# Kernel tuning notes

Measured on AMD Instinct MI355X. Metric: run time of the kernel, lower is better.

The kernel has to match this reference:

```python
import jax, jax.numpy as jnp
import numpy as np

NCAPS, NHIDDEN, NLAYER, ROUTIT = 8, 16, 2, 6
CUT = 5


def _normalize(v, axis):
    return v / jnp.maximum(jnp.linalg.norm(v, axis=axis, keepdims=True), 1e-12)


def _routing(x, nb_flat, k, max_iter, last):
    # x: [n, d] flat features, nb_flat: [n*m] neighbor ids (-1 = pad)
    n, d = x.shape
    dd = d // k
    m = nb_flat.shape[0] // n
    x3 = _normalize(x.reshape(n, k, dd), axis=2)              # [n,k,dd]
    x_c = jnp.concatenate([x3.reshape(n, d), jnp.zeros((1, d), x.dtype)], 0)  # [n+1,d]
    nbm = jnp.where(nb_flat < 0, n, nb_flat)
    z = x_c[nbm].reshape(n, m, k, dd)                         # neighbor gather
    u = None
    p = None
    for it in range(max_iter):
        p = jnp.zeros((n, m, k), x.dtype) if u is None else jnp.einsum('nmkc,nkc->nmk', z, u)
        p = jax.nn.softmax(p, axis=2)
        u = jnp.einsum('nmkc,nmk->nkc', z, p) + x3
        if it < max_iter - 1:
            u = _normalize(u, axis=2)
    if not last:
        return u.reshape(n, d)
    # meta-path aggregation (last layer)
    nb2 = nb_flat.reshape(n, m)
    nei_mask = (nb2 >= 0).astype(x.dtype)
    p1 = jnp.argmax(p, axis=2)                                # [n,m]
    A = jax.nn.one_hot(p1, k, dtype=x.dtype) * nei_mask[:, :, None]  # [n,m,k]
    Ai = A.transpose(2, 0, 1).astype(jnp.int32)               # [k,n,m]
    B = Ai * nb2[None].astype(jnp.int32) + (Ai - 1)           # nb where assigned, else -1
    B = jnp.concatenate([B, -jnp.ones((k, 1, m), jnp.int32)], axis=1)  # [k,n+1,m]
    mapB = jnp.where(B < 0, n, B)                             # -1 -> zero row n
    sel = mapB[:, :, :CUT]                                    # [k,n+1,CUT]
    x_c3 = x_c.reshape(n + 1, k, dd)
    gather_j = jax.vmap(lambda idx, xj: xj[idx], in_axes=(0, 1))  # over capsule j
    metas = []
    for i in range(k):
        # two-hop neighbors through capsule i then capsule j
        tmp = mapB[:, sel[i].reshape(-1), :CUT].reshape(k, n + 1, CUT * CUT)[:, :n]  # [k,n,25]
        hj = gather_j(tmp, x_c3)                               # [k,n,25,dd]
        metas.append(hj.mean(axis=2))                          # [k,n,dd]
    meta = jnp.stack(metas, 0)                                 # [i,j,n,dd]
    meta = meta.sum(axis=1).transpose(1, 0, 2)                 # sum over j -> [n,k,dd]
    meta = u + meta
    return u.reshape(n, d), meta.reshape(n, d)


def setup_inputs() -> dict:
    key = jax.random.key(0)
    ks = jax.random.split(key, 10)
    n, nfeat, nclass = 20000, 500, 16
    m = 32
    d = NCAPS * NHIDDEN
    return {
        'x': jax.random.normal(ks[0], (n, nfeat), jnp.float32),
        'nb': jax.random.randint(ks[1], (n, m), 0, n, jnp.int64),
        'pca_w': jax.random.normal(ks[2], (nfeat, d), jnp.float32) * 0.05,
        'pca_b': jax.random.normal(ks[3], (d,), jnp.float32) * 0.05,
        'ln_g': jnp.ones((NHIDDEN,), jnp.float32),
        'ln_b': jnp.zeros((NHIDDEN,), jnp.float32),
        'w_qs': jax.random.normal(ks[4], (NHIDDEN, NHIDDEN), jnp.float32) * 0.1,
        'w_ks': jax.random.normal(ks[5], (NHIDDEN, NHIDDEN), jnp.float32) * 0.1,
        'mlp_w': jax.random.normal(ks[6], (d, nclass), jnp.float32) * 0.05,
        'mlp_b': jax.random.normal(ks[7], (nclass,), jnp.float32) * 0.05,
    }


def reference(x, nb, pca_w, pca_b, ln_g, ln_b, w_qs, w_ks, mlp_w, mlp_b):
    k, dd = NCAPS, NHIDDEN
    n = x.shape[0]
    nb_flat = nb.reshape(-1)
    h = x @ pca_w + pca_b                                      # [n, d]
    h3 = h.reshape(n, k, dd)
    # Independence attention over capsules (only attn matters; output q is discarded)
    mu = h3.mean(-1, keepdims=True)
    var = ((h3 - mu) ** 2).mean(-1, keepdims=True)
    q = (h3 - mu) / jnp.sqrt(var + 1e-6) * ln_g + ln_b
    q = q @ w_qs                                               # [n,k,dd]
    kk = h3 @ w_ks
    temp = jnp.asarray(dd, x.dtype) ** 0.5
    attn = jax.nn.softmax(jnp.einsum('nqc,nkc->nqk', q / temp, kk), axis=-1)  # [n,k,k]
    off = 1.0 - jnp.eye(k, dtype=x.dtype)
    attn_loss = (attn * off).sum() / (off.sum() * n)
    h = jax.nn.relu(h3).reshape(n, k * dd)
    meta = None
    for layer in range(NLAYER):
        last = layer == NLAYER - 1
        if last:
            u, meta = _routing(h, nb_flat, k, ROUTIT, True)
        else:
            h = jax.nn.relu(_routing(h, nb_flat, k, ROUTIT, False))
    meta = jax.nn.relu(meta) @ mlp_w + mlp_b
    return jax.nn.log_softmax(meta, axis=1), attn_loss, meta
```

## Files before the change

kernel.cpp:

```cpp
#include <hip/hip_runtime.h>
#include <math.h>

#define NCAPS 8
#define DD    16
#define D     128
#define M     32
#define ROUTIT 6
#define CUT   5

__device__ __forceinline__ float wred16_sum(float v) {
    v += __shfl_xor(v, 1);
    v += __shfl_xor(v, 2);
    v += __shfl_xor(v, 4);
    v += __shfl_xor(v, 8);
    return v;
}

__device__ __forceinline__ void wave_sync_lds() {
    asm volatile("s_waitcnt lgkmcnt(0)" ::: "memory");
}

__device__ __forceinline__ void bar_lgkm() {
    asm volatile("s_waitcnt lgkmcnt(0)" ::: "memory");
    __builtin_amdgcn_s_barrier();
    asm volatile("" ::: "memory");
}

typedef _Float16 h2 __attribute__((ext_vector_type(2)));
union U32H2 { unsigned u; h2 h; };
__device__ __forceinline__ unsigned pack_h2(float a, float b) {
    U32H2 r; r.h.x = (_Float16)a; r.h.y = (_Float16)b; return r.u;
}
__device__ __forceinline__ h2 ash2(unsigned u) { U32H2 r; r.u = u; return r.h; }

__global__ __launch_bounds__(256) void pca_attn(
        const float* __restrict__ x, const float* __restrict__ w,
        const float* __restrict__ bias, const float* __restrict__ ln_g,
        const float* __restrict__ ln_b, const float* __restrict__ w_qs,
        const float* __restrict__ w_ks, unsigned* __restrict__ xc0H,
        unsigned* __restrict__ xc1H, float* __restrict__ partial,
        int n, int nfeat) {
    __shared__ alignas(16) unsigned char uS[20480];
    unsigned (*xs2)[36]  = (unsigned(*)[36])uS;
    unsigned (*ws2)[128] = (unsigned(*)[128])(uS + 1440);
    float (*ks)[8][20]   = (float(*)[8][20])uS;
    __shared__ alignas(16) float hs[32][132];
    __shared__ float wq[256], wk[256];
    __shared__ float red[4];
    const int tid = threadIdx.x;
    const int cg = tid & 31;
    const int rg = tid >> 5;
    const int row0 = blockIdx.x * 32;
    wq[tid] = w_qs[tid];
    wk[tid] = w_ks[tid];
    const float4 bi4 = *(const float4*)&bias[cg * 4];
    if (blockIdx.x == 0 && tid < 64) {
        xc0H[(size_t)n * 64 + tid] = 0u;
        xc1H[(size_t)n * 64 + tid] = 0u;
    }

    const int xr_r = tid / 5, xr_cf = tid % 5;
    const int wk0 = tid >> 5, wc0 = tid & 31;
    float4 xr{}, w0a{}, w0b{}, w1a{}, w1b{};

    {
        if (tid < 160) {
            int row = row0 + xr_r;
            xr = (row < n) ? *(const float4*)&x[(size_t)row * nfeat + xr_cf * 4]
                           : make_float4(0.f, 0.f, 0.f, 0.f);
        }
        w0a = *(const float4*)&w[(size_t)(2 * wk0) * 128 + wc0 * 4];
        w0b = *(const float4*)&w[(size_t)(2 * wk0 + 1) * 128 + wc0 * 4];
        if (tid < 64) {
            int kkp = 8 + (tid >> 5);
            w1a = *(const float4*)&w[(size_t)(2 * kkp) * 128 + wc0 * 4];
            w1b = *(const float4*)&w[(size_t)(2 * kkp + 1) * 128 + wc0 * 4];
        }
    }
    float acc[4][4] = {};
    const int ntile = nfeat / 20;
    for (int t = 0; t < ntile; ++t) {
        bar_lgkm();
        if (tid < 160) {
            xs2[xr_cf * 2 + 0][xr_r] = pack_h2(xr.x, xr.y);
            xs2[xr_cf * 2 + 1][xr_r] = pack_h2(xr.z, xr.w);
        }
        {
            uint4 pw;
            pw.x = pack_h2(w0a.x, w0b.x); pw.y = pack_h2(w0a.y, w0b.y);
            pw.z = pack_h2(w0a.z, w0b.z); pw.w = pack_h2(w0a.w, w0b.w);
            *(uint4*)&ws2[wk0][wc0 * 4] = pw;
        }
        if (tid < 64) {
            int kkp = 8 + (tid >> 5);
            uint4 pw;
            pw.x = pack_h2(w1a.x, w1b.x); pw.y = pack_h2(w1a.y, w1b.y);
            pw.z = pack_h2(w1a.z, w1b.z); pw.w = pack_h2(w1a.w, w1b.w);
            *(uint4*)&ws2[kkp][wc0 * 4] = pw;
        }
        if (t < ntile - 1) {
            int k0 = (t + 1) * 20;
            if (tid < 160) {
                int row = row0 + xr_r;
                xr = (row < n)
                    ? *(const float4*)&x[(size_t)row * nfeat + k0 + xr_cf * 4]
                    : make_float4(0.f, 0.f, 0.f, 0.f);
            }
            w0a = *(const float4*)&w[(size_t)(k0 + 2 * wk0) * 128 + wc0 * 4];
            w0b = *(const float4*)&w[(size_t)(k0 + 2 * wk0 + 1) * 128 + wc0 * 4];
            if (tid < 64) {
                int kkp = 8 + (tid >> 5);
                w1a = *(const float4*)&w[(size_t)(k0 + 2 * kkp) * 128 + wc0 * 4];
                w1b = *(const float4*)&w[(size_t)(k0 + 2 * kkp + 1) * 128 + wc0 * 4];
            }
        }
        bar_lgkm();
#pragma unroll
        for (int kkp = 0; kkp < 10; ++kkp) {
            uint4 av = *(const uint4*)&xs2[kkp][rg * 4];
            uint4 bv = *(const uint4*)&ws2[kkp][cg * 4];
            unsigned aa[4] = {av.x, av.y, av.z, av.w};
            unsigned bb[4] = {bv.x, bv.y, bv.z, bv.w};
#pragma unroll
            for (int i = 0; i < 4; ++i)
#pragma unroll
                for (int j = 0; j < 4; ++j)
                    acc[i][j] = __builtin_amdgcn_fdot2(ash2(aa[i]), ash2(bb[j]),
                                                       acc[i][j], false);
        }
    }
#pragma unroll
    for (int i = 0; i < 4; ++i)
        *(float4*)&hs[rg * 4 + i][cg * 4] =
            make_float4(acc[i][0] + bi4.x, acc[i][1] + bi4.y,
                        acc[i][2] + bi4.z, acc[i][3] + bi4.w);
    bar_lgkm();

    const int r = tid >> 3, kq = tid & 7;
    const int row = row0 + r;
    float hv[16], q[16], kk[16];
    if (row < n) {
#pragma unroll
        for (int i = 0; i < 4; ++i) {
            float4 f = *(const float4*)&hs[r][kq * 16 + i * 4];
            hv[i * 4 + 0] = f.x; hv[i * 4 + 1] = f.y;
            hv[i * 4 + 2] = f.z; hv[i * 4 + 3] = f.w;
        }
        float mu = 0.f;
#pragma unroll
        for (int c = 0; c < 16; ++c) mu += hv[c];
        mu *= (1.f / 16.f);
        float var = 0.f;
#pragma unroll
        for (int c = 0; c < 16; ++c) { float d = hv[c] - mu; var += d * d; }
        var *= (1.f / 16.f);
        float rstd = rsqrtf(var + 1e-6f);
        float qn[16];
#pragma unroll
        for (int c = 0; c < 16; ++c)
            qn[c] = (hv[c] - mu) * rstd * ln_g[c] + ln_b[c];
#pragma unroll
        for (int c = 0; c < 16; ++c) { q[c] = 0.f; kk[c] = 0.f; }
#pragma unroll
        for (int cp = 0; cp < 16; ++cp)
#pragma unroll
            for (int c = 0; c < 16; ++c) {
                q[c]  += qn[cp] * wq[cp * 16 + c];
                kk[c] += hv[cp] * wk[cp * 16 + c];
            }
#pragma unroll
        for (int c = 0; c < 16; ++c) q[c] *= 0.25f;
#pragma unroll
        for (int i = 0; i < 4; ++i)
            *(float4*)&ks[r][kq][i * 4] =
                make_float4(kk[i * 4], kk[i * 4 + 1], kk[i * 4 + 2], kk[i * 4 + 3]);
        float ss = 0.f;
        float rl[16];
#pragma unroll
        for (int c = 0; c < 16; ++c) { rl[c] = fmaxf(hv[c], 0.f); ss += rl[c] * rl[c]; }
        float inv = 1.f / fmaxf(sqrtf(ss), 1e-12f);
        unsigned* xo = xc0H + (size_t)row * 64 + kq * 8;
        uint4 pa, pb;
        pa.x = pack_h2(rl[0] * inv,  rl[1] * inv);
        pa.y = pack_h2(rl[2] * inv,  rl[3] * inv);
        pa.z = pack_h2(rl[4] * inv,  rl[5] * inv);
        pa.w = pack_h2(rl[6] * inv,  rl[7] * inv);
        pb.x = pack_h2(rl[8] * inv,  rl[9] * inv);
        pb.y = pack_h2(rl[10] * inv, rl[11] * inv);
        pb.z = pack_h2(rl[12] * inv, rl[13] * inv);
        pb.w = pack_h2(rl[14] * inv, rl[15] * inv);
        *(uint4*)&xo[0] = pa;
        *(uint4*)&xo[4] = pb;
    }
    bar_lgkm();

    float offd = 0.f;
    if (row < n) {
        float s[8];
#pragma unroll
        for (int j = 0; j < 8; ++j) {
            float d = 0.f;
#pragma unroll
            for (int i = 0; i < 4; ++i) {
                float4 f = *(const float4*)&ks[r][j][i * 4];
                d += q[i * 4] * f.x + q[i * 4 + 1] * f.y
                   + q[i * 4 + 2] * f.z + q[i * 4 + 3] * f.w;
            }
            s[j] = d;
        }
        float mx = s[0];
#pragma unroll
        for (int j = 1; j < 8; ++j) mx = fmaxf(mx, s[j]);
        float e[8], se = 0.f;
#pragma unroll
        for (int j = 0; j < 8; ++j) { e[j] = __expf(s[j] - mx); se += e[j]; }
        float rse = 1.f / se;
#pragma unroll
        for (int j = 0; j < 8; ++j)
            if (j != kq) offd += e[j] * rse;
    }
    offd += __shfl_xor(offd, 1);
    offd += __shfl_xor(offd, 2);
    offd += __shfl_xor(offd, 4);
    offd += __shfl_xor(offd, 8);
    offd += __shfl_xor(offd, 16);
    offd += __shfl_xor(offd, 32);
    int lane = tid & 63, wid = tid >> 6;
    if (lane == 0) red[wid] = offd;
    bar_lgkm();
    if (tid == 0) partial[blockIdx.x] = red[0] + red[1] + red[2] + red[3];
}

__global__ __launch_bounds__(256) void reduce_kernel(
        const float* __restrict__ partial, float* __restrict__ acc, int npart) {
    __shared__ float red[4];
    const int t = threadIdx.x;
    float s = 0.f;
    for (int i = t; i < npart; i += 256) s += partial[i];
    s += __shfl_xor(s, 1);  s += __shfl_xor(s, 2);
    s += __shfl_xor(s, 4);  s += __shfl_xor(s, 8);
    s += __shfl_xor(s, 16); s += __shfl_xor(s, 32);
    if ((t & 63) == 0) red[t >> 6] = s;
    __syncthreads();
    if (t == 0) acc[0] = red[0] + red[1] + red[2] + red[3];
}

template <bool LAST>
__global__ __launch_bounds__(64, 4) void routing_kernel(
        const unsigned* __restrict__ xcH,
        const int* __restrict__ nb,
        float* __restrict__ outF,
        unsigned* __restrict__ outH,
        int* __restrict__ amax, int n) {
    __shared__ alignas(16) unsigned char sbuf[8192];
    uint2* zsu = (uint2*)sbuf;
    uint2* usu = (uint2*)sbuf;
    float* pT  = (float*)(sbuf + 320);
    const int l = threadIdx.x;
    const int v = blockIdx.x;
    const int m  = l & 31;
    const int kh = l >> 5;

    float4 x3;
    {
        int sm = l >> 1, sh = l & 1;
        int src = 0;
        if (l < M) {
            int nbv = nb[(size_t)v * M + l];
            src = (nbv < 0) ? n : nbv;
        }
        int srow = __shfl(src, sm);
        const uint4* g = (const uint4*)(xcH + (size_t)srow * 64 + sh * 32);
        uint2 xv = *(const uint2*)(xcH + (size_t)v * 64 + m * 2);
        uint4 zb[8];
#pragma unroll
        for (int i = 0; i < 8; ++i) zb[i] = g[i];
        {
            h2 xlo = ash2(xv.x), xhi = ash2(xv.y);
            x3 = make_float4((float)xlo.x, (float)xlo.y,
                             (float)xhi.x, (float)xhi.y);
        }
#pragma unroll
        for (int i = 0; i < 8; ++i) {
            int f0 = sh * 16 + 2 * i;
            zsu[sm * 32 + (f0 ^ sm)]       = make_uint2(zb[i].x, zb[i].y);
            zsu[sm * 32 + ((f0 + 1) ^ sm)] = make_uint2(zb[i].z, zb[i].w);
        }
    }
    wave_sync_lds();

    uint2 zpr[16];
#pragma unroll
    for (int idx = 0; idx < 16; ++idx) {
        int f = kh * 16 + idx;
        zpr[idx] = zsu[m * 32 + (f ^ m)];
    }
    uint2 zu[16];
#pragma unroll
    for (int j = 0; j < 16; ++j) {
        int r = kh * 16 + j;
        zu[j] = zsu[r * 32 + (m ^ r)];
    }
    wave_sync_lds();

    {
        float4 a = make_float4(0.f, 0.f, 0.f, 0.f);
#pragma unroll
        for (int j = 0; j < 16; ++j) {
            h2 lo = ash2(zu[j].x), hi = ash2(zu[j].y);
            a.x += (float)lo.x; a.y += (float)lo.y;
            a.z += (float)hi.x; a.w += (float)hi.y;
        }
        a.x += __shfl_xor(a.x, 32); a.y += __shfl_xor(a.y, 32);
        a.z += __shfl_xor(a.z, 32); a.w += __shfl_xor(a.w, 32);
        a.x = a.x * 0.125f + x3.x;  a.y = a.y * 0.125f + x3.y;
        a.z = a.z * 0.125f + x3.z;  a.w = a.w * 0.125f + x3.w;
        float ss = a.x * a.x + a.y * a.y + a.z * a.z + a.w * a.w;
        ss += __shfl_xor(ss, 1); ss += __shfl_xor(ss, 2);
        float inv = 1.f / fmaxf(sqrtf(ss), 1e-12f);
        if (l < 32)
            usu[(m >> 2) * 5 + (m & 3)] =
                make_uint2(pack_h2(a.x * inv, a.y * inv),
                           pack_h2(a.z * inv, a.w * inv));
    }
    wave_sync_lds();

    for (int it = 1; it < ROUTIT; ++it) {
        float pr[4];
#pragma unroll
        for (int j = 0; j < 4; ++j) {
            float s = 0.f;
            const uint2* uk = &usu[(kh * 4 + j) * 5];
#pragma unroll
            for (int c2 = 0; c2 < 4; ++c2) {
                uint2 zz = zpr[j * 4 + c2];
                uint2 uu = uk[c2];
                s = __builtin_amdgcn_fdot2(ash2(zz.x), ash2(uu.x), s, false);
                s = __builtin_amdgcn_fdot2(ash2(zz.y), ash2(uu.y), s, false);
            }
            pr[j] = s;
        }
        float po[4];
#pragma unroll
        for (int j = 0; j < 4; ++j) po[j] = __shfl_xor(pr[j], 32);
        if (LAST && it == ROUTIT - 1) {
            float p8[8];
#pragma unroll
            for (int j = 0; j < 4; ++j) {
                p8[kh * 4 + j] = pr[j];
                p8[(kh ^ 1) * 4 + j] = po[j];
            }
            float bv = p8[0]; int bi = 0;
#pragma unroll
            for (int k2 = 1; k2 < 8; ++k2)
                if (p8[k2] > bv) { bv = p8[k2]; bi = k2; }
            if (l < 32) amax[(size_t)v * M + m] = bi;
        }
        float er[4], S = 0.f;
#pragma unroll
        for (int j = 0; j < 4; ++j) { er[j] = __expf(pr[j]); S += er[j]; }
#pragma unroll
        for (int j = 0; j < 4; ++j) S += __expf(po[j]);
        float rS = 1.f / S;
#pragma unroll
        for (int j = 0; j < 4; ++j)
            pT[(kh * 4 + j) * 36 + m] = er[j] * rS;
        wave_sync_lds();

        float pk[16];
        {
            const int k2 = m >> 2;
#pragma unroll
            for (int j4 = 0; j4 < 4; ++j4) {
                float4 pp = *(const float4*)&pT[k2 * 36 + kh * 16 + j4 * 4];
                pk[j4 * 4 + 0] = pp.x; pk[j4 * 4 + 1] = pp.y;
                pk[j4 * 4 + 2] = pp.z; pk[j4 * 4 + 3] = pp.w;
            }
        }
        float4 a = make_float4(0.f, 0.f, 0.f, 0.f);
#pragma unroll
        for (int j = 0; j < 16; ++j) {
            h2 lo = ash2(zu[j].x), hi = ash2(zu[j].y);
            a.x += (float)lo.x * pk[j]; a.y += (float)lo.y * pk[j];
            a.z += (float)hi.x * pk[j]; a.w += (float)hi.y * pk[j];
        }
        a.x += __shfl_xor(a.x, 32); a.y += __shfl_xor(a.y, 32);
        a.z += __shfl_xor(a.z, 32); a.w += __shfl_xor(a.w, 32);
        a.x += x3.x; a.y += x3.y; a.z += x3.z; a.w += x3.w;

        if (it < ROUTIT - 1) {
            float ss = a.x * a.x + a.y * a.y + a.z * a.z + a.w * a.w;
            ss += __shfl_xor(ss, 1); ss += __shfl_xor(ss, 2);
            float inv = 1.f / fmaxf(sqrtf(ss), 1e-12f);
            if (l < 32)
                usu[(m >> 2) * 5 + (m & 3)] =
                    make_uint2(pack_h2(a.x * inv, a.y * inv),
                               pack_h2(a.z * inv, a.w * inv));
            wave_sync_lds();
        } else if (LAST) {
            if (l < 32) ((float4*)(outF + (size_t)v * D))[m] = a;
        } else {
            float r0 = fmaxf(a.x, 0.f), r1 = fmaxf(a.y, 0.f);
            float r2 = fmaxf(a.z, 0.f), r3 = fmaxf(a.w, 0.f);
            float ss = r0 * r0 + r1 * r1 + r2 * r2 + r3 * r3;
            ss += __shfl_xor(ss, 1); ss += __shfl_xor(ss, 2);
            float inv = 1.f / fmaxf(sqrtf(ss), 1e-12f);
            if (l < 32)
                *(uint2*)(outH + (size_t)v * 64 + m * 2) =
                    make_uint2(pack_h2(r0 * inv, r1 * inv),
                               pack_h2(r2 * inv, r3 * inv));
        }
    }
}

__global__ __launch_bounds__(256) void s2_kernel(
        const unsigned* __restrict__ xc1H, const int* __restrict__ nb,
        const int* __restrict__ amax, float* __restrict__ s2, int n) {
    int idx = blockIdx.x * 256 + threadIdx.x;
    if (idx >= n * 16) return;
    int w = idx >> 4, c = idx & 15;
    float s = 0.f;
#pragma unroll
    for (int b = 0; b < CUT; ++b) {
        int t  = nb[(size_t)w * M + b];
        int jj = amax[(size_t)w * M + b];
        int im = (t < 0) ? n : t;
        unsigned uv = xc1H[(size_t)im * 64 + jj * 8 + (c >> 1)];
        h2 hh = ash2(uv);
        s += (c & 1) ? (float)hh.y : (float)hh.x;
    }
    s2[idx] = s;
}

__global__ __launch_bounds__(256) void meta_kernel(
        const float* __restrict__ u1, const float* __restrict__ s2,
        const int* __restrict__ nb, const int* __restrict__ amax,
        const float* __restrict__ mlp_w, const float* __restrict__ mlp_b,
        const float* __restrict__ attn_acc, float* __restrict__ d_out, int n) {
    __shared__ float Wl[128 * 16];
    __shared__ float accs[16][132];
    const int t = threadIdx.x;
#pragma unroll
    for (int i = 0; i < 8; ++i) Wl[t + i * 256] = mlp_w[t + i * 256];
    const int g = t >> 4, c = t & 15;
    const int v = blockIdx.x * 16 + g;
    if (blockIdx.x == 0 && t == 0)
        d_out[(size_t)n * 16] = attn_acc[0] * (1.f / (56.f * (float)n));
    if (v < n) {
#pragma unroll
        for (int i = 0; i < 8; ++i) accs[g][i * 16 + c] = 0.f;
        for (int a = 0; a < CUT; ++a) {
            int w = nb[(size_t)v * M + a];
            if (w < 0) continue;
            int i = amax[(size_t)v * M + a];
            accs[g][i * 16 + c] += s2[(size_t)w * 16 + c];
        }
#pragma unroll
        for (int i = 0; i < 8; ++i) {
            float meta = u1[(size_t)v * D + i * 16 + c] + accs[g][i * 16 + c] * (1.f / 25.f);
            accs[g][i * 16 + c] = fmaxf(meta, 0.f);
        }
    }
    __syncthreads();
    if (v < n) {
        float o = mlp_b[c];
#pragma unroll
        for (int dd = 0; dd < 128; ++dd) o += accs[g][dd] * Wl[dd * 16 + c];
        float mx = o;
        mx = fmaxf(mx, __shfl_xor(mx, 1));
        mx = fmaxf(mx, __shfl_xor(mx, 2));
        mx = fmaxf(mx, __shfl_xor(mx, 4));
        mx = fmaxf(mx, __shfl_xor(mx, 8));
        float e = __expf(o - mx);
        float se = wred16_sum(e);
        float ls = (o - mx) - logf(se);
        d_out[(size_t)v * 16 + c] = ls;
        d_out[(size_t)n * 16 + 1 + (size_t)v * 16 + c] = o;
    }
}

extern "C" void kernel_launch(void* const* d_in, const int* in_sizes, int n_in,
                              void* d_out, int out_size, void* d_ws, size_t ws_size,
                              hipStream_t stream) {
    const float* x     = (const float*)d_in[0];
    const int*   nb    = (const int*)d_in[1];
    const float* pca_w = (const float*)d_in[2];
    const float* pca_b = (const float*)d_in[3];
    const float* ln_g  = (const float*)d_in[4];
    const float* ln_b  = (const float*)d_in[5];
    const float* w_qs  = (const float*)d_in[6];
    const float* w_ks  = (const float*)d_in[7];
    const float* mlp_w = (const float*)d_in[8];
    const float* mlp_b = (const float*)d_in[9];
    float* out = (float*)d_out;

    const int d = 128;
    const int nfeat = in_sizes[2] / d;
    const int n = in_sizes[0] / nfeat;
    const int nblk = (n + 31) / 32;

    float* bufA = (float*)d_ws;
    unsigned* bufB = (unsigned*)(bufA + (size_t)n * d);
    unsigned* bufC = bufB + (size_t)(n + 1) * 64;
    float* acc  = (float*)(bufC + (size_t)(n + 1) * 64);
    int* amax = (int*)bufB;
    float* s2 = (float*)((int*)bufB + (size_t)n * M);
    float* partial = (float*)bufC;

    pca_attn<<<nblk, 256, 0, stream>>>(x, pca_w, pca_b, ln_g, ln_b, w_qs, w_ks,
                                       bufB, bufC, partial, n, nfeat);
    reduce_kernel<<<1, 256, 0, stream>>>(partial, acc, nblk);
    routing_kernel<false><<<n, 64, 0, stream>>>(bufB, nb, nullptr, bufC, nullptr, n);
    routing_kernel<true><<<n, 64, 0, stream>>>(bufC, nb, bufA, nullptr, amax, n);
    s2_kernel<<<(n * 16 + 255) / 256, 256, 0, stream>>>(bufC, nb, amax, s2, n);
    meta_kernel<<<(n + 15) / 16, 256, 0, stream>>>(bufA, s2, nb, amax, mlp_w, mlp_b, acc, out, n);
}
```

Measured before the change: 236.6 us.

## Fuse s2 computation into last routing kernel and fold reduction into meta kernel

Computes the s2 neighbor-feature sums inside the last routing kernel, reading the gathered neighbor rows already held in LDS instead of re-gathering them from global memory in a separate kernel. The attention-loss partial reduction moves into the first block of meta_kernel, so the standalone reduce kernel goes away. Together these remove two launches and a global gather pass. The LDS layout is shifted so usu and pT no longer overlap the z buffer, which keeps z intact for reuse, and a serial 64-lane reduction is added to one meta block.

New measurement: 236.1 us. Within noise of the previous version (-0.2%).

```diff
diff --git a/kernel.cpp b/kernel.cpp
--- a/kernel.cpp
+++ b/kernel.cpp
@@ -231,31 +231,19 @@
     if (tid == 0) partial[blockIdx.x] = red[0] + red[1] + red[2] + red[3];
 }
 
-__global__ __launch_bounds__(256) void reduce_kernel(
-        const float* __restrict__ partial, float* __restrict__ acc, int npart) {
-    __shared__ float red[4];
-    const int t = threadIdx.x;
-    float s = 0.f;
-    for (int i = t; i < npart; i += 256) s += partial[i];
-    s += __shfl_xor(s, 1);  s += __shfl_xor(s, 2);
-    s += __shfl_xor(s, 4);  s += __shfl_xor(s, 8);
-    s += __shfl_xor(s, 16); s += __shfl_xor(s, 32);
-    if ((t & 63) == 0) red[t >> 6] = s;
-    __syncthreads();
-    if (t == 0) acc[0] = red[0] + red[1] + red[2] + red[3];
-}
-
 template <bool LAST>
 __global__ __launch_bounds__(64, 4) void routing_kernel(
         const unsigned* __restrict__ xcH,
         const int* __restrict__ nb,
         float* __restrict__ outF,
         unsigned* __restrict__ outH,
-        int* __restrict__ amax, int n) {
+        int* __restrict__ amax,
+        float* __restrict__ s2out,
+        int n) {
     __shared__ alignas(16) unsigned char sbuf[8192];
     uint2* zsu = (uint2*)sbuf;
-    uint2* usu = (uint2*)sbuf;
-    float* pT  = (float*)(sbuf + 320);
+    uint2* usu = (uint2*)(sbuf + 6656);
+    float* pT  = (float*)(sbuf + 6976);
     const int l = threadIdx.x;
     const int v = blockIdx.x;
     const int m  = l & 31;
@@ -325,6 +313,7 @@
     }
     wave_sync_lds();
 
+    int my_amax = 0;
     for (int it = 1; it < ROUTIT; ++it) {
         float pr[4];
 #pragma unroll
@@ -354,6 +343,7 @@
 #pragma unroll
             for (int k2 = 1; k2 < 8; ++k2)
                 if (p8[k2] > bv) { bv = p8[k2]; bi = k2; }
+            my_amax = bi;
             if (l < 32) amax[(size_t)v * M + m] = bi;
         }
         float er[4], S = 0.f;
@@ -399,6 +389,18 @@
             wave_sync_lds();
         } else if (LAST) {
             if (l < 32) ((float4*)(outF + (size_t)v * D))[m] = a;
+            int c = l & 15;
+            float s = 0.f;
+#pragma unroll
+            for (int b = 0; b < CUT; ++b) {
+                int jjb = __shfl(my_amax, b);
+                int slot = jjb * 4 + (c >> 2);
+                uint2 zz = zsu[b * 32 + (slot ^ b)];
+                unsigned word = (c & 2) ? zz.y : zz.x;
+                h2 hh = ash2(word);
+                s += (c & 1) ? (float)hh.y : (float)hh.x;
+            }
+            if (l < 16) s2out[(size_t)v * 16 + c] = s;
         } else {
             float r0 = fmaxf(a.x, 0.f), r1 = fmaxf(a.y, 0.f);
             float r2 = fmaxf(a.z, 0.f), r3 = fmaxf(a.w, 0.f);
@@ -413,30 +415,12 @@
     }
 }
 
-__global__ __launch_bounds__(256) void s2_kernel(
-        const unsigned* __restrict__ xc1H, const int* __restrict__ nb,
-        const int* __restrict__ amax, float* __restrict__ s2, int n) {
-    int idx = blockIdx.x * 256 + threadIdx.x;
-    if (idx >= n * 16) return;
-    int w = idx >> 4, c = idx & 15;
-    float s = 0.f;
-#pragma unroll
-    for (int b = 0; b < CUT; ++b) {
-        int t  = nb[(size_t)w * M + b];
-        int jj = amax[(size_t)w * M + b];
-        int im = (t < 0) ? n : t;
-        unsigned uv = xc1H[(size_t)im * 64 + jj * 8 + (c >> 1)];
-        h2 hh = ash2(uv);
-        s += (c & 1) ? (float)hh.y : (float)hh.x;
-    }
-    s2[idx] = s;
-}
-
 __global__ __launch_bounds__(256) void meta_kernel(
         const float* __restrict__ u1, const float* __restrict__ s2,
         const int* __restrict__ nb, const int* __restrict__ amax,
         const float* __restrict__ mlp_w, const float* __restrict__ mlp_b,
-        const float* __restrict__ attn_acc, float* __restrict__ d_out, int n) {
+        const float* __restrict__ partial, float* __restrict__ d_out,
+        int n, int npart) {
     __shared__ float Wl[128 * 16];
     __shared__ float accs[16][132];
     const int t = threadIdx.x;
@@ -444,8 +428,14 @@
     for (int i = 0; i < 8; ++i) Wl[t + i * 256] = mlp_w[t + i * 256];
     const int g = t >> 4, c = t & 15;
     const int v = blockIdx.x * 16 + g;
-    if (blockIdx.x == 0 && t == 0)
-        d_out[(size_t)n * 16] = attn_acc[0] * (1.f / (56.f * (float)n));
+    if (blockIdx.x == 0 && t < 64) {
+        float s = 0.f;
+        for (int i = t; i < npart; i += 64) s += partial[i];
+        s += __shfl_xor(s, 1);  s += __shfl_xor(s, 2);
+        s += __shfl_xor(s, 4);  s += __shfl_xor(s, 8);
+        s += __shfl_xor(s, 16); s += __shfl_xor(s, 32);
+        if (t == 0) d_out[(size_t)n * 16] = s * (1.f / (56.f * (float)n));
+    }
     if (v < n) {
 #pragma unroll
         for (int i = 0; i < 8; ++i) accs[g][i * 16 + c] = 0.f;
@@ -502,16 +492,16 @@
     float* bufA = (float*)d_ws;
     unsigned* bufB = (unsigned*)(bufA + (size_t)n * d);
     unsigned* bufC = bufB + (size_t)(n + 1) * 64;
-    float* acc  = (float*)(bufC + (size_t)(n + 1) * 64);
+    float* partial = (float*)(bufC + (size_t)(n + 1) * 64);
     int* amax = (int*)bufB;
     float* s2 = (float*)((int*)bufB + (size_t)n * M);
-    float* partial = (float*)bufC;
 
     pca_attn<<<nblk, 256, 0, stream>>>(x, pca_w, pca_b, ln_g, ln_b, w_qs, w_ks,
                                        bufB, bufC, partial, n, nfeat);
-    reduce_kernel<<<1, 256, 0, stream>>>(partial, acc, nblk);
-    routing_kernel<false><<<n, 64, 0, stream>>>(bufB, nb, nullptr, bufC, nullptr, n);
-    routing_kernel<true><<<n, 64, 0, stream>>>(bufC, nb, bufA, nullptr, amax, n);
-    s2_kernel<<<(n * 16 + 255) / 256, 256, 0, stream>>>(bufC, nb, amax, s2, n);
-    meta_kernel<<<(n + 15) / 16, 256, 0, stream>>>(bufA, s2, nb, amax, mlp_w, mlp_b, acc, out, n);
-}
+    routing_kernel<false><<<n, 64, 0, stream>>>(bufB, nb, nullptr, bufC,
+                                                nullptr, nullptr, n);
+    routing_kernel<true><<<n, 64, 0, stream>>>(bufC, nb, bufA, nullptr,
+                                               amax, s2, n);
+    meta_kernel<<<(n + 15) / 16, 256, 0, stream>>>(bufA, s2, nb, amax, mlp_w,
+                                                   mlp_b, partial, out, n, nblk);
+}
```
